# Kernel optimization log

Measured on AMD Instinct MI355X. Metric: run time of the kernel, lower is better.

The kernel has to match this reference:

```python
import jax, jax.numpy as jnp
import numpy as np

N_NODES = 8192
N_EDGES = 524288
N_PAIRS = 262144
N_TYPES = 86


def _gcn_conv(x, W, b, src, dst, n):
    # PyG GCNConv: transform, add self-loops, symmetric degree normalization,
    # scatter-add aggregation at destination nodes.
    xw = x @ W  # [N, F_out]
    loop = jnp.arange(n, dtype=src.dtype)
    s = jnp.concatenate([src, loop])
    d = jnp.concatenate([dst, loop])
    deg = jax.ops.segment_sum(jnp.ones(d.shape, xw.dtype), d, num_segments=n)
    dinv = jnp.where(deg > 0, jax.lax.rsqrt(deg), 0.0)  # deg^{-1/2}, 0 for isolated
    coef = dinv[s] * dinv[d]  # [E+N]
    out = jax.ops.segment_sum(xw[s] * coef[:, None], d, num_segments=n)
    return out + b


def setup_inputs() -> dict:
    key = jax.random.key(0)
    ks = jax.random.split(key, 10)
    x = jax.random.normal(ks[0], (N_NODES, N_NODES), dtype=jnp.float32)
    edge_index = jax.random.randint(ks[1], (2, N_EDGES), 0, N_NODES, dtype=jnp.int32)
    drug1_idx = jax.random.randint(ks[2], (N_PAIRS,), 0, N_NODES, dtype=jnp.int32)
    drug2_idx = jax.random.randint(ks[3], (N_PAIRS,), 0, N_NODES, dtype=jnp.int32)
    W1 = jax.random.normal(ks[4], (N_NODES, 128), dtype=jnp.float32) / np.sqrt(N_NODES)
    b1 = jnp.zeros((128,), jnp.float32)
    W2 = jax.random.normal(ks[5], (128, 64), dtype=jnp.float32) / np.sqrt(128.0)
    b2 = jnp.zeros((64,), jnp.float32)
    Wfc = jax.random.normal(ks[6], (128, N_TYPES), dtype=jnp.float32) / np.sqrt(128.0)
    bfc = jnp.zeros((N_TYPES,), jnp.float32)
    return {"x": x, "edge_index": edge_index, "drug1_idx": drug1_idx,
            "drug2_idx": drug2_idx, "W1": W1, "b1": b1, "W2": W2, "b2": b2,
            "Wfc": Wfc, "bfc": bfc}


def reference(x, edge_index, drug1_idx, drug2_idx, W1, b1, W2, b2, Wfc, bfc):
    n = x.shape[0]
    src, dst = edge_index[0], edge_index[1]
    h = jax.nn.relu(_gcn_conv(x, W1, b1, src, dst, n))
    # dropout p=0.3 is identity at inference (training=False)
    h = jax.nn.relu(_gcn_conv(h, W2, b2, src, dst, n))
    combined = jnp.concatenate([h[drug1_idx], h[drug2_idx]], axis=1)  # [P, 128]
    return jax.nn.sigmoid(combined @ Wfc + bfc)
```

## Files before the change

### kernel.cpp

```cpp
#include <hip/hip_runtime.h>
#include <math.h>
#include <stdint.h>
#include <stddef.h>

#define N_NODES 8192
#define N_EDGES 524288
#define N_PAIRS 262144
#define N_TYPES 86
#define F1 128
#define F2 64

typedef unsigned short ushort_t;
typedef unsigned int uint_t;
typedef __attribute__((ext_vector_type(8))) short bfrag;
typedef __attribute__((ext_vector_type(4))) float ffrag;

typedef __attribute__((address_space(3))) char lds_char;
typedef __attribute__((address_space(1))) const char g_char;

__device__ __forceinline__ void gload16(const void* g, void* l) {
  __builtin_amdgcn_global_load_lds((const g_char*)g, (lds_char*)l, 16, 0, 0);
}

__device__ inline ushort_t f2bf(float f) {
  uint_t u = __float_as_uint(f);
  uint_t r = u + 0x7fffu + ((u >> 16) & 1u);
  return (ushort_t)(r >> 16);
}
__device__ inline float bf2f(ushort_t h) {
  return __uint_as_float(((uint_t)h) << 16);
}


__global__ void zero_k(int* __restrict__ p) {
  p[blockIdx.x * 256 + threadIdx.x] = 0;
}

__global__ void count_deg_k(const int* __restrict__ dst, int* __restrict__ cnt) {
  int e = blockIdx.x * blockDim.x + threadIdx.x;
  if (e < N_EDGES) atomicAdd(&cnt[dst[e]], 1);
}

__global__ void scan_k(const int* __restrict__ cnt, int* __restrict__ rp,
                       int* __restrict__ fill, float* __restrict__ dinv) {
  __shared__ int s[1024];
  int t = threadIdx.x;
  int v[8];
  int sum = 0;
#pragma unroll
  for (int i = 0; i < 8; i++) {
    v[i] = cnt[t * 8 + i];
    dinv[t * 8 + i] = 1.0f / sqrtf((float)(v[i] + 1));
    sum += v[i];
  }
  s[t] = sum;
  __syncthreads();
  for (int off = 1; off < 1024; off <<= 1) {
    int add = (t >= off) ? s[t - off] : 0;
    __syncthreads();
    s[t] += add;
    __syncthreads();
  }
  int excl = s[t] - sum;
#pragma unroll
  for (int i = 0; i < 8; i++) {
    rp[t * 8 + i] = excl;
    fill[t * 8 + i] = excl;
    excl += v[i];
  }
  if (t == 1023) rp[N_NODES] = excl;
}

__global__ void scatter_k(const int* __restrict__ src, const int* __restrict__ dst,
                          int* fill, int* __restrict__ csr) {
  int e = blockIdx.x * blockDim.x + threadIdx.x;
  if (e < N_EDGES) {
    int d = dst[e];
    int pos = atomicAdd(&fill[d], 1);
    csr[pos] = src[e];
  }
}


__global__ __launch_bounds__(256) void w1t_k(const float* __restrict__ W1,
                                             ushort_t* __restrict__ W1t) {
  __shared__ ushort_t lh[32 * 65];
  int tid = threadIdx.x;
  int k0 = blockIdx.x * 64;
  int n0 = blockIdx.y * 32;
#pragma unroll
  for (int i = 0; i < 8; i++) {
    int c = tid + 256 * i;
    int kr = c >> 5, nc = c & 31;
    lh[nc * 65 + kr] = f2bf(W1[(size_t)(k0 + kr) * F1 + n0 + nc]);
  }
  __syncthreads();
  {
    int c = tid;
    int nr = c >> 3, kc = c & 7;
    uint4 u;
    u.x = (uint_t)lh[nr * 65 + kc * 8 + 0] | ((uint_t)lh[nr * 65 + kc * 8 + 1] << 16);
    u.y = (uint_t)lh[nr * 65 + kc * 8 + 2] | ((uint_t)lh[nr * 65 + kc * 8 + 3] << 16);
    u.z = (uint_t)lh[nr * 65 + kc * 8 + 4] | ((uint_t)lh[nr * 65 + kc * 8 + 5] << 16);
    u.w = (uint_t)lh[nr * 65 + kc * 8 + 6] | ((uint_t)lh[nr * 65 + kc * 8 + 7] << 16);
    *(uint4*)(W1t + (size_t)(n0 + nr) * N_NODES + k0 + kc * 8) = u;
  }
}


#define ALDS 0
#define BLDS(b) (16384 + (b) * 8192)

#define SCHED0 __builtin_amdgcn_sched_barrier(0)
#define WAITVM(N)  do { asm volatile("s_waitcnt vmcnt(" #N ")" ::: "memory"); SCHED0; } while (0)
#define WAITVML(N) do { asm volatile("s_waitcnt vmcnt(" #N ") lgkmcnt(0)" ::: "memory"); SCHED0; } while (0)

__global__ __launch_bounds__(256, 2) void gemm1_mfma_k(const float* __restrict__ x,
                                                       const ushort_t* __restrict__ W1t,
                                                       float* __restrict__ part, int kspan) {
  __shared__ __align__(16) char lds[32768];
  int tid = threadIdx.x;
  int wave = tid >> 6, lane = tid & 63;
  int wr = wave >> 1, wc = wave & 1;
  int lrow = lane & 15, kgrp = lane >> 4;
  int m_blk = blockIdx.y * 128;
  int kbase = blockIdx.x * kspan;
  int ktiles = kspan >> 5;
  int s0 = (5 * blockIdx.y + 3 * blockIdx.x) & (ktiles - 1);

  int ar = tid >> 1, aq = tid & 1;
  const float* abase = x + (size_t)(m_blk + ar) * N_NODES + aq * 16;

  int bq = wave;
  int b_row = bq * 32 + (lane >> 2);
  int b_kel = ((lane & 3) ^ ((lane >> 2) & 3)) << 3;

  ffrag acc[4][4];
#pragma unroll
  for (int mi = 0; mi < 4; mi++)
#pragma unroll
    for (int ni = 0; ni < 4; ni++) acc[mi][ni] = (ffrag)(0.0f);

  float4 av[4];

#define LOADA(K0)                                                                    \
  {                                                                                  \
    const float* p_ = abase + (K0);                                                  \
    av[0] = *(const float4*)(p_ + 0);                                                \
    av[1] = *(const float4*)(p_ + 4);                                                \
    av[2] = *(const float4*)(p_ + 8);                                                \
    av[3] = *(const float4*)(p_ + 12);                                               \
  }

#define ISSUE_B(K0, BSEL)                                                            \
  {                                                                                  \
    _Pragma("unroll") for (int i = 0; i < 2; i++) {                                  \
      const ushort_t* gp = W1t + (size_t)(b_row + i * 16) * N_NODES + (K0) + b_kel;  \
      gload16(gp, lds + BLDS(BSEL) + bq * 2048 + i * 1024);                          \
    }                                                                                \
  }

#define STOREA()                                                                     \
  {                                                                                  \
    float f[16];                                                                     \
    f[0]=av[0].x; f[1]=av[0].y; f[2]=av[0].z; f[3]=av[0].w;                          \
    f[4]=av[1].x; f[5]=av[1].y; f[6]=av[1].z; f[7]=av[1].w;                          \
    f[8]=av[2].x; f[9]=av[2].y; f[10]=av[2].z; f[11]=av[2].w;                        \
    f[12]=av[3].x; f[13]=av[3].y; f[14]=av[3].z; f[15]=av[3].w;                      \
    ushort_t h[16], l[16];                                                           \
    _Pragma("unroll") for (int j = 0; j < 16; j++) {                                 \
      h[j] = f2bf(f[j]);                                                             \
      l[j] = f2bf(f[j] - bf2f(h[j]));                                                \
    }                                                                                \
    uint4 H0, H1, L0, L1;                                                            \
    H0.x=(uint_t)h[0]|((uint_t)h[1]<<16);  H0.y=(uint_t)h[2]|((uint_t)h[3]<<16);     \
    H0.z=(uint_t)h[4]|((uint_t)h[5]<<16);  H0.w=(uint_t)h[6]|((uint_t)h[7]<<16);     \
    H1.x=(uint_t)h[8]|((uint_t)h[9]<<16);  H1.y=(uint_t)h[10]|((uint_t)h[11]<<16);   \
    H1.z=(uint_t)h[12]|((uint_t)h[13]<<16); H1.w=(uint_t)h[14]|((uint_t)h[15]<<16);  \
    L0.x=(uint_t)l[0]|((uint_t)l[1]<<16);  L0.y=(uint_t)l[2]|((uint_t)l[3]<<16);     \
    L0.z=(uint_t)l[4]|((uint_t)l[5]<<16);  L0.w=(uint_t)l[6]|((uint_t)l[7]<<16);     \
    L1.x=(uint_t)l[8]|((uint_t)l[9]<<16);  L1.y=(uint_t)l[10]|((uint_t)l[11]<<16);   \
    L1.z=(uint_t)l[12]|((uint_t)l[13]<<16); L1.w=(uint_t)l[14]|((uint_t)l[15]<<16);  \
    uint_t rb = ar * 128, rx = ar & 7;                                               \
    *(uint4*)(lds + ALDS + rb + (((2*aq)   ^ rx) << 4)) = H0;                        \
    *(uint4*)(lds + ALDS + rb + (((2*aq+1) ^ rx) << 4)) = H1;                        \
    *(uint4*)(lds + ALDS + rb + (((4+2*aq) ^ rx) << 4)) = L0;                        \
    *(uint4*)(lds + ALDS + rb + (((5+2*aq) ^ rx) << 4)) = L1;                        \
  }

#define COMPUTE(BSEL)                                                                \
  {                                                                                  \
    bfrag bh[4];                                                                     \
    _Pragma("unroll") for (int ni = 0; ni < 4; ni++) {                               \
      int brow = wc * 64 + ni * 16 + lrow;                                           \
      uint_t boff = brow * 64 + ((kgrp ^ (brow & 3)) << 4);                          \
      bh[ni] = *(const bfrag*)(lds + BLDS(BSEL) + boff);                             \
    }                                                                                \
    _Pragma("unroll") for (int mi = 0; mi < 4; mi++) {                               \
      int arow = wr * 64 + mi * 16 + lrow;                                           \
      uint_t rb = arow * 128, rx = arow & 7;                                         \
      bfrag ah = *(const bfrag*)(lds + ALDS + rb + ((kgrp ^ rx) << 4));              \
      bfrag al = *(const bfrag*)(lds + ALDS + rb + (((4 + kgrp) ^ rx) << 4));        \
      _Pragma("unroll") for (int ni = 0; ni < 4; ni++) {                             \
        acc[mi][ni] = __builtin_amdgcn_mfma_f32_16x16x32_bf16(ah, bh[ni], acc[mi][ni], 0, 0, 0); \
        acc[mi][ni] = __builtin_amdgcn_mfma_f32_16x16x32_bf16(al, bh[ni], acc[mi][ni], 0, 0, 0); \
      }                                                                              \
    }                                                                                \
  }

  LOADA(kbase + (s0 << 5));
  ISSUE_B(kbase + (s0 << 5), 0);
  WAITVM(2);
  STOREA();
  WAITVML(0);
  __builtin_amdgcn_s_barrier();
  SCHED0;

  int sp = s0;
  for (int s = 0; s < ktiles; ++s) {
    int more = (s + 1 < ktiles);
    int spn = sp + 1; if (spn == ktiles) spn = 0;
    if (more) {
      int k0n = kbase + (spn << 5);
      LOADA(k0n);
      SCHED0;
      ISSUE_B(k0n, (s + 1) & 1);
      SCHED0;
    }
    __builtin_amdgcn_s_setprio(1);
    COMPUTE(s & 1);
    __builtin_amdgcn_s_setprio(0);
    __builtin_amdgcn_s_barrier();
    SCHED0;
    if (more) {
      WAITVM(2);
      STOREA();
      WAITVML(0);
      __builtin_amdgcn_s_barrier();
      SCHED0;
    }
    sp = spn;
  }

  float* outp = part + (size_t)blockIdx.x * (N_NODES * F1);
#pragma unroll
  for (int mi = 0; mi < 4; mi++) {
#pragma unroll
    for (int ni = 0; ni < 4; ni++) {
      int col = wc * 64 + ni * 16 + lrow;
#pragma unroll
      for (int r = 0; r < 4; r++) {
        int row = m_blk + wr * 64 + mi * 16 + kgrp * 4 + r;
        outp[(size_t)row * F1 + col] = acc[mi][ni][r];
      }
    }
  }
#undef LOADA
#undef ISSUE_B
#undef STOREA
#undef COMPUTE
}

__global__ void reduceS_k(const float* __restrict__ part, float* __restrict__ xw1, int S) {
  int i = blockIdx.x * blockDim.x + threadIdx.x;
  float4 a = ((const float4*)part)[i];
  for (int s = 1; s < S; s++) {
    float4 b = ((const float4*)(part + (size_t)s * N_NODES * F1))[i];
    a.x += b.x; a.y += b.y; a.z += b.z; a.w += b.w;
  }
  ((float4*)xw1)[i] = a;
}


template <int F>
__global__ void agg_k(const float* __restrict__ xw, const int* __restrict__ csr,
                      const int* __restrict__ rp, const float* __restrict__ dinv,
                      const float* __restrict__ bias, float* __restrict__ hout) {
  int node = blockIdx.x;
  int f = threadIdx.x;
  __shared__ int sidx[F];
  __shared__ float sdv[F];
  int beg = rp[node], end = rp[node + 1];
  float acc = 0.f;
  for (int base = beg; base < end; base += F) {
    int n = end - base;
    if (n > F) n = F;
    __syncthreads();
    if (f < n) {
      int s = csr[base + f];
      sidx[f] = s;
      sdv[f] = dinv[s];
    }
    __syncthreads();
    for (int i = 0; i < n; i++) acc += xw[(size_t)sidx[i] * F + f] * sdv[i];
  }
  float dv = dinv[node];
  float v = (acc + xw[(size_t)node * F + f] * dv) * dv + bias[f];
  hout[(size_t)node * F + f] = v > 0.f ? v : 0.f;
}


__global__ __launch_bounds__(256) void gemm2_k(const float* __restrict__ h1,
                                               const float* __restrict__ W2,
                                               float* __restrict__ xw2) {
  __shared__ float W2s[F1 * F2];
  __shared__ float As[16 * F1];
  int tid = threadIdx.x;
  int r0 = blockIdx.x * 16;
#pragma unroll
  for (int j = 0; j < 8; j++)
    ((float4*)W2s)[tid + 256 * j] = ((const float4*)W2)[tid + 256 * j];
#pragma unroll
  for (int j = 0; j < 2; j++)
    ((float4*)As)[tid + 256 * j] = ((const float4*)(h1 + (size_t)r0 * F1))[tid + 256 * j];
  __syncthreads();
  int r = tid >> 4, c4 = tid & 15;
  float4 acc = make_float4(0.f, 0.f, 0.f, 0.f);
#pragma unroll 8
  for (int k = 0; k < F1; k++) {
    float a = As[r * F1 + k];
    float4 bv = *(float4*)&W2s[k * F2 + 4 * c4];
    acc.x += a * bv.x; acc.y += a * bv.y; acc.z += a * bv.z; acc.w += a * bv.w;
  }
  *(float4*)&xw2[(size_t)(r0 + r) * F2 + 4 * c4] = acc;
}


__global__ void pboth_k(const float* __restrict__ h2, const float* __restrict__ Wfc,
                        float* __restrict__ P) {
  __shared__ float hs[64 * 16];
  int tid = threadIdx.x;
  int r0 = blockIdx.x * 16;
  for (int idx = tid; idx < 256; idx += 192) {
    int row = idx >> 4, k4 = idx & 15;
    float4 h = *(const float4*)&h2[(size_t)(r0 + row) * F2 + 4 * k4];
    hs[(4 * k4 + 0) * 16 + row] = h.x;
    hs[(4 * k4 + 1) * 16 + row] = h.y;
    hs[(4 * k4 + 2) * 16 + row] = h.z;
    hs[(4 * k4 + 3) * 16 + row] = h.w;
  }
  __syncthreads();
  if (tid < 172) {
    int half = tid < 86 ? 0 : 1;
    int j = tid - 86 * half;
    const float* wp = Wfc + (size_t)(64 * half) * N_TYPES + j;
    float acc[16];
#pragma unroll
    for (int r = 0; r < 16; r++) acc[r] = 0.f;
    for (int k = 0; k < 64; k++) {
      float w = wp[(size_t)k * N_TYPES];
      const float* hk = &hs[k * 16];
#pragma unroll
      for (int r = 0; r < 16; r++) acc[r] += hk[r] * w;
    }
#pragma unroll
    for (int r = 0; r < 16; r++) P[(size_t)(r0 + r) * 172 + tid] = acc[r];
  }
}


__global__ void final_k(const float* __restrict__ P, const int* __restrict__ d1,
                        const int* __restrict__ d2, const float* __restrict__ bfc,
                        float* __restrict__ out) {
  int gid = blockIdx.x * blockDim.x + threadIdx.x;
  if (gid >= N_PAIRS * 43) return;
  int p = gid / 43;
  int j = gid - p * 43;
  int a = d1[p], b = d2[p];
  float2 v1 = *(const float2*)&P[(size_t)a * 172 + 2 * j];
  float2 v2 = *(const float2*)&P[(size_t)b * 172 + 86 + 2 * j];
  float2 bb = *(const float2*)&bfc[2 * j];
  float z0 = v1.x + v2.x + bb.x;
  float z1 = v1.y + v2.y + bb.y;
  float2 o;
  o.x = 1.0f / (1.0f + expf(-z0));
  o.y = 1.0f / (1.0f + expf(-z1));
  *(float2*)&out[(size_t)p * 86 + 2 * j] = o;
}


extern "C" void kernel_launch(void* const* d_in, const int* in_sizes, int n_in,
                              void* d_out, int out_size, void* d_ws, size_t ws_size,
                              hipStream_t stream) {
  const float* x   = (const float*)d_in[0];
  const int*   ei  = (const int*)d_in[1];
  const int*   d1  = (const int*)d_in[2];
  const int*   d2  = (const int*)d_in[3];
  const float* W1  = (const float*)d_in[4];
  const float* b1  = (const float*)d_in[5];
  const float* W2  = (const float*)d_in[6];
  const float* b2  = (const float*)d_in[7];
  const float* Wfc = (const float*)d_in[8];
  const float* bfc = (const float*)d_in[9];
  float* out = (float*)d_out;

  const int* esrc = ei;
  const int* edst = ei + N_EDGES;

  char* w = (char*)d_ws;
  size_t off = 0;
  auto alloc = [&](size_t bytes) -> char* {
    char* p = w + off;
    off += (bytes + 255) & ~(size_t)255;
    return p;
  };
  int*      cnt  = (int*)alloc((size_t)N_NODES * 4);
  float*    dinv = (float*)alloc((size_t)N_NODES * 4);
  int*      rp   = (int*)alloc((size_t)(N_NODES + 1) * 4);
  int*      fill = (int*)alloc((size_t)N_NODES * 4);
  int*      csr  = (int*)alloc((size_t)N_EDGES * 4);
  ushort_t* W1t  = (ushort_t*)alloc((size_t)N_NODES * F1 * 2);
  float*    h1   = (float*)alloc((size_t)N_NODES * F1 * 4);
  float*    xw2  = (float*)alloc((size_t)N_NODES * F2 * 4);
  float*    h2   = (float*)alloc((size_t)N_NODES * F2 * 4);
  float*    P    = (float*)alloc((size_t)N_NODES * 172 * 4);

  size_t partBytes = (size_t)N_NODES * F1 * 4;
  int S = 8;
  while (S > 1 && off + (size_t)S * partBytes > ws_size) S >>= 1;
  float* part = (float*)alloc((size_t)S * partBytes);
  float* xw1 = part;
  if (off > ws_size) return;

  zero_k<<<N_NODES / 256, 256, 0, stream>>>(cnt);
  count_deg_k<<<N_EDGES / 256, 256, 0, stream>>>(edst, cnt);
  scan_k<<<1, 1024, 0, stream>>>(cnt, rp, fill, dinv);
  scatter_k<<<N_EDGES / 256, 256, 0, stream>>>(esrc, edst, fill, csr);

  w1t_k<<<dim3(N_NODES / 64, F1 / 32), 256, 0, stream>>>(W1, W1t);
  gemm1_mfma_k<<<dim3(S, N_NODES / 128), 256, 0, stream>>>(x, W1t, part, N_NODES / S);
  if (S > 1)
    reduceS_k<<<(N_NODES * F1 / 4) / 256, 256, 0, stream>>>(part, xw1, S);
  agg_k<F1><<<N_NODES, F1, 0, stream>>>(xw1, csr, rp, dinv, b1, h1);

  gemm2_k<<<N_NODES / 16, 256, 0, stream>>>(h1, W2, xw2);
  agg_k<F2><<<N_NODES, F2, 0, stream>>>(xw2, csr, rp, dinv, b2, h2);

  pboth_k<<<N_NODES / 16, 192, 0, stream>>>(h2, Wfc, P);
  final_k<<<(N_PAIRS * 43 + 255) / 256, 256, 0, stream>>>(P, d1, d2, bfc, out);
}
```

Before: 251.5 us.

## Drop bf16 low-part correction in GEMM1 and widen aggregation per thread

GEMM1 now converts x to a single bf16 value instead of a hi/lo split, halving MFMA count and A-tile LDS, with a padded row stride replacing the XOR swizzle. Lower LDS use allows raising launch bounds to 4 blocks per CU. The aggregation kernel uses 64-thread blocks with float2 loads for the 128-feature layer. The trade-off is reduced precision of the first GEMM (bf16 inputs) and possible LDS bank conflicts from the new padding.

```diff
diff --git a/kernel.cpp b/kernel.cpp
--- a/kernel.cpp
+++ b/kernel.cpp
@@ -109,16 +109,16 @@
 
 
 #define ALDS 0
-#define BLDS(b) (16384 + (b) * 8192)
+#define BLDS(b) (10240 + (b) * 8192)
 
 #define SCHED0 __builtin_amdgcn_sched_barrier(0)
 #define WAITVM(N)  do { asm volatile("s_waitcnt vmcnt(" #N ")" ::: "memory"); SCHED0; } while (0)
 #define WAITVML(N) do { asm volatile("s_waitcnt vmcnt(" #N ") lgkmcnt(0)" ::: "memory"); SCHED0; } while (0)
 
-__global__ __launch_bounds__(256, 2) void gemm1_mfma_k(const float* __restrict__ x,
+__global__ __launch_bounds__(256, 4) void gemm1_mfma_k(const float* __restrict__ x,
                                                        const ushort_t* __restrict__ W1t,
                                                        float* __restrict__ part, int kspan) {
-  __shared__ __align__(16) char lds[32768];
+  __shared__ __align__(16) char lds[26624];
   int tid = threadIdx.x;
   int wave = tid >> 6, lane = tid & 63;
   int wr = wave >> 1, wc = wave & 1;
@@ -162,30 +162,19 @@
 
 #define STOREA()                                                                     \
   {                                                                                  \
-    float f[16];                                                                     \
-    f[0]=av[0].x; f[1]=av[0].y; f[2]=av[0].z; f[3]=av[0].w;                          \
-    f[4]=av[1].x; f[5]=av[1].y; f[6]=av[1].z; f[7]=av[1].w;                          \
-    f[8]=av[2].x; f[9]=av[2].y; f[10]=av[2].z; f[11]=av[2].w;                        \
-    f[12]=av[3].x; f[13]=av[3].y; f[14]=av[3].z; f[15]=av[3].w;                      \
-    ushort_t h[16], l[16];                                                           \
-    _Pragma("unroll") for (int j = 0; j < 16; j++) {                                 \
-      h[j] = f2bf(f[j]);                                                             \
-      l[j] = f2bf(f[j] - bf2f(h[j]));                                                \
-    }                                                                                \
-    uint4 H0, H1, L0, L1;                                                            \
+    ushort_t h[16];                                                                  \
+    h[0]=f2bf(av[0].x); h[1]=f2bf(av[0].y); h[2]=f2bf(av[0].z); h[3]=f2bf(av[0].w);  \
+    h[4]=f2bf(av[1].x); h[5]=f2bf(av[1].y); h[6]=f2bf(av[1].z); h[7]=f2bf(av[1].w);  \
+    h[8]=f2bf(av[2].x); h[9]=f2bf(av[2].y); h[10]=f2bf(av[2].z); h[11]=f2bf(av[2].w);\
+    h[12]=f2bf(av[3].x); h[13]=f2bf(av[3].y); h[14]=f2bf(av[3].z); h[15]=f2bf(av[3].w);\
+    uint4 H0, H1;                                                                    \
     H0.x=(uint_t)h[0]|((uint_t)h[1]<<16);  H0.y=(uint_t)h[2]|((uint_t)h[3]<<16);     \
     H0.z=(uint_t)h[4]|((uint_t)h[5]<<16);  H0.w=(uint_t)h[6]|((uint_t)h[7]<<16);     \
     H1.x=(uint_t)h[8]|((uint_t)h[9]<<16);  H1.y=(uint_t)h[10]|((uint_t)h[11]<<16);   \
     H1.z=(uint_t)h[12]|((uint_t)h[13]<<16); H1.w=(uint_t)h[14]|((uint_t)h[15]<<16);  \
-    L0.x=(uint_t)l[0]|((uint_t)l[1]<<16);  L0.y=(uint_t)l[2]|((uint_t)l[3]<<16);     \
-    L0.z=(uint_t)l[4]|((uint_t)l[5]<<16);  L0.w=(uint_t)l[6]|((uint_t)l[7]<<16);     \
-    L1.x=(uint_t)l[8]|((uint_t)l[9]<<16);  L1.y=(uint_t)l[10]|((uint_t)l[11]<<16);   \
-    L1.z=(uint_t)l[12]|((uint_t)l[13]<<16); L1.w=(uint_t)l[14]|((uint_t)l[15]<<16);  \
-    uint_t rb = ar * 128, rx = ar & 7;                                               \
-    *(uint4*)(lds + ALDS + rb + (((2*aq)   ^ rx) << 4)) = H0;                        \
-    *(uint4*)(lds + ALDS + rb + (((2*aq+1) ^ rx) << 4)) = H1;                        \
-    *(uint4*)(lds + ALDS + rb + (((4+2*aq) ^ rx) << 4)) = L0;                        \
-    *(uint4*)(lds + ALDS + rb + (((5+2*aq) ^ rx) << 4)) = L1;                        \
+    uint_t rb = ar * 80 + aq * 32;                                                   \
+    *(uint4*)(lds + ALDS + rb) = H0;                                                 \
+    *(uint4*)(lds + ALDS + rb + 16) = H1;                                            \
   }
 
 #define COMPUTE(BSEL)                                                                \
@@ -198,12 +187,9 @@
     }                                                                                \
     _Pragma("unroll") for (int mi = 0; mi < 4; mi++) {                               \
       int arow = wr * 64 + mi * 16 + lrow;                                           \
-      uint_t rb = arow * 128, rx = arow & 7;                                         \
-      bfrag ah = *(const bfrag*)(lds + ALDS + rb + ((kgrp ^ rx) << 4));              \
-      bfrag al = *(const bfrag*)(lds + ALDS + rb + (((4 + kgrp) ^ rx) << 4));        \
+      bfrag ah = *(const bfrag*)(lds + ALDS + arow * 80 + kgrp * 16);                \
       _Pragma("unroll") for (int ni = 0; ni < 4; ni++) {                             \
         acc[mi][ni] = __builtin_amdgcn_mfma_f32_16x16x32_bf16(ah, bh[ni], acc[mi][ni], 0, 0, 0); \
-        acc[mi][ni] = __builtin_amdgcn_mfma_f32_16x16x32_bf16(al, bh[ni], acc[mi][ni], 0, 0, 0); \
       }                                                                              \
     }                                                                                \
   }
@@ -278,13 +264,13 @@
                       const float* __restrict__ bias, float* __restrict__ hout) {
   int node = blockIdx.x;
   int f = threadIdx.x;
-  __shared__ int sidx[F];
-  __shared__ float sdv[F];
+  __shared__ int sidx[64];
+  __shared__ float sdv[64];
   int beg = rp[node], end = rp[node + 1];
-  float acc = 0.f;
-  for (int base = beg; base < end; base += F) {
+  float ax = 0.f, ay = 0.f;
+  for (int base = beg; base < end; base += 64) {
     int n = end - base;
-    if (n > F) n = F;
+    if (n > 64) n = 64;
     __syncthreads();
     if (f < n) {
       int s = csr[base + f];
@@ -292,11 +278,31 @@
       sdv[f] = dinv[s];
     }
     __syncthreads();
-    for (int i = 0; i < n; i++) acc += xw[(size_t)sidx[i] * F + f] * sdv[i];
+    if constexpr (F == 128) {
+      for (int i = 0; i < n; i++) {
+        float dv = sdv[i];
+        float2 v = ((const float2*)&xw[(size_t)sidx[i] * F])[f];
+        ax += v.x * dv;
+        ay += v.y * dv;
+      }
+    } else {
+      for (int i = 0; i < n; i++) ax += xw[(size_t)sidx[i] * F + f] * sdv[i];
+    }
   }
   float dv = dinv[node];
-  float v = (acc + xw[(size_t)node * F + f] * dv) * dv + bias[f];
-  hout[(size_t)node * F + f] = v > 0.f ? v : 0.f;
+  if constexpr (F == 128) {
+    float2 sv = ((const float2*)&xw[(size_t)node * F])[f];
+    float2 bb = ((const float2*)bias)[f];
+    float vx = (ax + sv.x * dv) * dv + bb.x;
+    float vy = (ay + sv.y * dv) * dv + bb.y;
+    float2 o;
+    o.x = vx > 0.f ? vx : 0.f;
+    o.y = vy > 0.f ? vy : 0.f;
+    ((float2*)&hout[(size_t)node * F])[f] = o;
+  } else {
+    float v = (ax + xw[(size_t)node * F + f] * dv) * dv + bias[f];
+    hout[(size_t)node * F + f] = v > 0.f ? v : 0.f;
+  }
 }
 
 
@@ -431,10 +437,10 @@
   gemm1_mfma_k<<<dim3(S, N_NODES / 128), 256, 0, stream>>>(x, W1t, part, N_NODES / S);
   if (S > 1)
     reduceS_k<<<(N_NODES * F1 / 4) / 256, 256, 0, stream>>>(part, xw1, S);
-  agg_k<F1><<<N_NODES, F1, 0, stream>>>(xw1, csr, rp, dinv, b1, h1);
+  agg_k<F1><<<N_NODES, 64, 0, stream>>>(xw1, csr, rp, dinv, b1, h1);
 
   gemm2_k<<<N_NODES / 16, 256, 0, stream>>>(h1, W2, xw2);
-  agg_k<F2><<<N_NODES, F2, 0, stream>>>(xw2, csr, rp, dinv, b2, h2);
+  agg_k<F2><<<N_NODES, 64, 0, stream>>>(xw2, csr, rp, dinv, b2, h2);
 
   pboth_k<<<N_NODES / 16, 192, 0, stream>>>(h2, Wfc, P);
   final_k<<<(N_PAIRS * 43 + 255) / 256, 256, 0, stream>>>(P, d1, d2, bfc, out);
```

Measured after the change: 264.8 us. 5.3% more time.

## Load A fragments directly to registers with single-bf16 conversion in GEMM1

Applied to the files above, without the earlier changes.

The GEMM1 kernel no longer splits x into hi/lo bf16 parts staged through LDS. Each wave now loads its A fragments straight into registers, converts them with packed bf16 conversion instructions, and issues one MFMA per tile instead of two. A is double-buffered in registers across a 2-stage unrolled loop, which halves LDS usage and MFMA work and removes the LDS write path. The cost is lower precision, since the bf16 residual term is dropped, plus extra registers for the prefetch buffers. The loop also assumes an even tile count and wraps past the end, loading tiles that are never used.

```diff
diff --git a/kernel.cpp b/kernel.cpp
--- a/kernel.cpp
+++ b/kernel.cpp
@@ -13,6 +13,7 @@
 typedef unsigned short ushort_t;
 typedef unsigned int uint_t;
 typedef __attribute__((ext_vector_type(8))) short bfrag;
+typedef __attribute__((ext_vector_type(4))) uint_t ufrag;
 typedef __attribute__((ext_vector_type(4))) float ffrag;
 
 typedef __attribute__((address_space(3))) char lds_char;
@@ -29,6 +30,17 @@
 }
 __device__ inline float bf2f(ushort_t h) {
   return __uint_as_float(((uint_t)h) << 16);
+}
+
+__device__ __forceinline__ bfrag cvtfrag(float4 a, float4 b) {
+  uint_t h0, h1, h2, h3;
+  asm("v_cvt_pk_bf16_f32 %0, %1, %2" : "=v"(h0) : "v"(a.x), "v"(a.y));
+  asm("v_cvt_pk_bf16_f32 %0, %1, %2" : "=v"(h1) : "v"(a.z), "v"(a.w));
+  asm("v_cvt_pk_bf16_f32 %0, %1, %2" : "=v"(h2) : "v"(b.x), "v"(b.y));
+  asm("v_cvt_pk_bf16_f32 %0, %1, %2" : "=v"(h3) : "v"(b.z), "v"(b.w));
+  ufrag u;
+  u.x = h0; u.y = h1; u.z = h2; u.w = h3;
+  return __builtin_bit_cast(bfrag, u);
 }
 
 
@@ -108,17 +120,15 @@
 }
 
 
-#define ALDS 0
-#define BLDS(b) (16384 + (b) * 8192)
+#define BLDS(b) ((b) * 8192)
 
 #define SCHED0 __builtin_amdgcn_sched_barrier(0)
 #define WAITVM(N)  do { asm volatile("s_waitcnt vmcnt(" #N ")" ::: "memory"); SCHED0; } while (0)
-#define WAITVML(N) do { asm volatile("s_waitcnt vmcnt(" #N ") lgkmcnt(0)" ::: "memory"); SCHED0; } while (0)
 
 __global__ __launch_bounds__(256, 2) void gemm1_mfma_k(const float* __restrict__ x,
                                                        const ushort_t* __restrict__ W1t,
                                                        float* __restrict__ part, int kspan) {
-  __shared__ __align__(16) char lds[32768];
+  __shared__ __align__(16) char lds[16384];
   int tid = threadIdx.x;
   int wave = tid >> 6, lane = tid & 63;
   int wr = wave >> 1, wc = wave & 1;
@@ -128,8 +138,10 @@
   int ktiles = kspan >> 5;
   int s0 = (5 * blockIdx.y + 3 * blockIdx.x) & (ktiles - 1);
 
-  int ar = tid >> 1, aq = tid & 1;
-  const float* abase = x + (size_t)(m_blk + ar) * N_NODES + aq * 16;
+  const float* ap0 = x + (size_t)(m_blk + wr * 64 + 0 * 16 + lrow) * N_NODES + kgrp * 8;
+  const float* ap1 = x + (size_t)(m_blk + wr * 64 + 1 * 16 + lrow) * N_NODES + kgrp * 8;
+  const float* ap2 = x + (size_t)(m_blk + wr * 64 + 2 * 16 + lrow) * N_NODES + kgrp * 8;
+  const float* ap3 = x + (size_t)(m_blk + wr * 64 + 3 * 16 + lrow) * N_NODES + kgrp * 8;
 
   int bq = wave;
   int b_row = bq * 32 + (lane >> 2);
@@ -141,15 +153,27 @@
 #pragma unroll
     for (int ni = 0; ni < 4; ni++) acc[mi][ni] = (ffrag)(0.0f);
 
-  float4 av[4];
-
-#define LOADA(K0)                                                                    \
+  float4 sP[8], sQ[8];
+  bfrag afr[4];
+
+#define ISSUE_A(KO, SET)                                                             \
   {                                                                                  \
-    const float* p_ = abase + (K0);                                                  \
-    av[0] = *(const float4*)(p_ + 0);                                                \
-    av[1] = *(const float4*)(p_ + 4);                                                \
-    av[2] = *(const float4*)(p_ + 8);                                                \
-    av[3] = *(const float4*)(p_ + 12);                                               \
+    SET[0] = *(const float4*)(ap0 + (KO));                                           \
+    SET[1] = *(const float4*)(ap0 + (KO) + 4);                                       \
+    SET[2] = *(const float4*)(ap1 + (KO));                                           \
+    SET[3] = *(const float4*)(ap1 + (KO) + 4);                                       \
+    SET[4] = *(const float4*)(ap2 + (KO));                                           \
+    SET[5] = *(const float4*)(ap2 + (KO) + 4);                                       \
+    SET[6] = *(const float4*)(ap3 + (KO));                                           \
+    SET[7] = *(const float4*)(ap3 + (KO) + 4);                                       \
+  }
+
+#define CONV(SET)                                                                    \
+  {                                                                                  \
+    afr[0] = cvtfrag(SET[0], SET[1]);                                                \
+    afr[1] = cvtfrag(SET[2], SET[3]);                                                \
+    afr[2] = cvtfrag(SET[4], SET[5]);                                                \
+    afr[3] = cvtfrag(SET[6], SET[7]);                                                \
   }
 
 #define ISSUE_B(K0, BSEL)                                                            \
@@ -158,34 +182,6 @@
       const ushort_t* gp = W1t + (size_t)(b_row + i * 16) * N_NODES + (K0) + b_kel;  \
       gload16(gp, lds + BLDS(BSEL) + bq * 2048 + i * 1024);                          \
     }                                                                                \
-  }
-
-#define STOREA()                                                                     \
-  {                                                                                  \
-    float f[16];                                                                     \
-    f[0]=av[0].x; f[1]=av[0].y; f[2]=av[0].z; f[3]=av[0].w;                          \
-    f[4]=av[1].x; f[5]=av[1].y; f[6]=av[1].z; f[7]=av[1].w;                          \
-    f[8]=av[2].x; f[9]=av[2].y; f[10]=av[2].z; f[11]=av[2].w;                        \
-    f[12]=av[3].x; f[13]=av[3].y; f[14]=av[3].z; f[15]=av[3].w;                      \
-    ushort_t h[16], l[16];                                                           \
-    _Pragma("unroll") for (int j = 0; j < 16; j++) {                                 \
-      h[j] = f2bf(f[j]);                                                             \
-      l[j] = f2bf(f[j] - bf2f(h[j]));                                                \
-    }                                                                                \
-    uint4 H0, H1, L0, L1;                                                            \
-    H0.x=(uint_t)h[0]|((uint_t)h[1]<<16);  H0.y=(uint_t)h[2]|((uint_t)h[3]<<16);     \
-    H0.z=(uint_t)h[4]|((uint_t)h[5]<<16);  H0.w=(uint_t)h[6]|((uint_t)h[7]<<16);     \
-    H1.x=(uint_t)h[8]|((uint_t)h[9]<<16);  H1.y=(uint_t)h[10]|((uint_t)h[11]<<16);   \
-    H1.z=(uint_t)h[12]|((uint_t)h[13]<<16); H1.w=(uint_t)h[14]|((uint_t)h[15]<<16);  \
-    L0.x=(uint_t)l[0]|((uint_t)l[1]<<16);  L0.y=(uint_t)l[2]|((uint_t)l[3]<<16);     \
-    L0.z=(uint_t)l[4]|((uint_t)l[5]<<16);  L0.w=(uint_t)l[6]|((uint_t)l[7]<<16);     \
-    L1.x=(uint_t)l[8]|((uint_t)l[9]<<16);  L1.y=(uint_t)l[10]|((uint_t)l[11]<<16);   \
-    L1.z=(uint_t)l[12]|((uint_t)l[13]<<16); L1.w=(uint_t)l[14]|((uint_t)l[15]<<16);  \
-    uint_t rb = ar * 128, rx = ar & 7;                                               \
-    *(uint4*)(lds + ALDS + rb + (((2*aq)   ^ rx) << 4)) = H0;                        \
-    *(uint4*)(lds + ALDS + rb + (((2*aq+1) ^ rx) << 4)) = H1;                        \
-    *(uint4*)(lds + ALDS + rb + (((4+2*aq) ^ rx) << 4)) = L0;                        \
-    *(uint4*)(lds + ALDS + rb + (((5+2*aq) ^ rx) << 4)) = L1;                        \
   }
 
 #define COMPUTE(BSEL)                                                                \
@@ -197,49 +193,60 @@
       bh[ni] = *(const bfrag*)(lds + BLDS(BSEL) + boff);                             \
     }                                                                                \
     _Pragma("unroll") for (int mi = 0; mi < 4; mi++) {                               \
-      int arow = wr * 64 + mi * 16 + lrow;                                           \
-      uint_t rb = arow * 128, rx = arow & 7;                                         \
-      bfrag ah = *(const bfrag*)(lds + ALDS + rb + ((kgrp ^ rx) << 4));              \
-      bfrag al = *(const bfrag*)(lds + ALDS + rb + (((4 + kgrp) ^ rx) << 4));        \
       _Pragma("unroll") for (int ni = 0; ni < 4; ni++) {                             \
-        acc[mi][ni] = __builtin_amdgcn_mfma_f32_16x16x32_bf16(ah, bh[ni], acc[mi][ni], 0, 0, 0); \
-        acc[mi][ni] = __builtin_amdgcn_mfma_f32_16x16x32_bf16(al, bh[ni], acc[mi][ni], 0, 0, 0); \
+        acc[mi][ni] = __builtin_amdgcn_mfma_f32_16x16x32_bf16(afr[mi], bh[ni], acc[mi][ni], 0, 0, 0); \
       }                                                                              \
     }                                                                                \
   }
 
-  LOADA(kbase + (s0 << 5));
-  ISSUE_B(kbase + (s0 << 5), 0);
-  WAITVM(2);
-  STOREA();
-  WAITVML(0);
+#define NXT(p) ((p) + 1 == ktiles ? 0 : (p) + 1)
+
+  int p1 = s0;
+  int p2 = NXT(p1);
+  ISSUE_A(kbase + (p1 << 5), sP);
+  SCHED0;
+  ISSUE_B(kbase + (p1 << 5), 0);
+  SCHED0;
+  ISSUE_A(kbase + (p2 << 5), sQ);
+  WAITVM(10);
+  CONV(sP);
+  WAITVM(8);
   __builtin_amdgcn_s_barrier();
   SCHED0;
 
-  int sp = s0;
-  for (int s = 0; s < ktiles; ++s) {
-    int more = (s + 1 < ktiles);
-    int spn = sp + 1; if (spn == ktiles) spn = 0;
-    if (more) {
-      int k0n = kbase + (spn << 5);
-      LOADA(k0n);
-      SCHED0;
-      ISSUE_B(k0n, (s + 1) & 1);
-      SCHED0;
+  for (int it = 0; it < ktiles; it += 2) {
+    {
+      int pB = NXT(p1), pA = NXT(pB);
+      ISSUE_B(kbase + (pB << 5), 1);
+      SCHED0;
+      ISSUE_A(kbase + (pA << 5), sP);
+      SCHED0;
+      __builtin_amdgcn_s_setprio(1);
+      COMPUTE(0);
+      __builtin_amdgcn_s_setprio(0);
+      WAITVM(10);
+      CONV(sQ);
+      WAITVM(8);
+      __builtin_amdgcn_s_barrier();
+      SCHED0;
+      p1 = pB;
     }
-    __builtin_amdgcn_s_setprio(1);
-    COMPUTE(s & 1);
-    __builtin_amdgcn_s_setprio(0);
-    __builtin_amdgcn_s_barrier();
-    SCHED0;
-    if (more) {
-      WAITVM(2);
-      STOREA();
-      WAITVML(0);
+    {
+      int pB = NXT(p1), pA = NXT(pB);
+      ISSUE_B(kbase + (pB << 5), 0);
+      SCHED0;
+      ISSUE_A(kbase + (pA << 5), sQ);
+      SCHED0;
+      __builtin_amdgcn_s_setprio(1);
+      COMPUTE(1);
+      __builtin_amdgcn_s_setprio(0);
+      WAITVM(10);
+      CONV(sP);
+      WAITVM(8);
       __builtin_amdgcn_s_barrier();
       SCHED0;
+      p1 = pB;
     }
-    sp = spn;
   }
 
   float* outp = part + (size_t)blockIdx.x * (N_NODES * F1);
@@ -255,10 +262,11 @@
       }
     }
   }
-#undef LOADA
+#undef ISSUE_A
+#undef CONV
 #undef ISSUE_B
-#undef STOREA
 #undef COMPUTE
+#undef NXT
 }
 
 __global__ void reduceS_k(const float* __restrict__ part, float* __restrict__ xw1, int S) {
```

Result: slower. 265.5 us (+5.6%).
